# Optimization experiments

Measured on AMD Instinct MI355X. Metric: run time of the kernel, lower is better.

Reference implementation:

```python
import jax, jax.numpy as jnp
import numpy as np

D_IN = 1024
D_OUT = 1024

def setup_inputs() -> dict:
    key = jax.random.key(0)
    ks = jax.random.split(key, 7)
    s = 1.0 / np.sqrt(D_IN)
    x = jax.random.normal(ks[0], (4, 2048, D_IN), dtype=jnp.float32)
    Wq = jax.random.uniform(ks[1], (D_IN, D_OUT), jnp.float32, -s, s)
    Wk = jax.random.uniform(ks[2], (D_IN, D_OUT), jnp.float32, -s, s)
    Wv = jax.random.uniform(ks[3], (D_IN, D_OUT), jnp.float32, -s, s)
    bq = jax.random.uniform(ks[4], (D_OUT,), jnp.float32, -s, s)
    bk = jax.random.uniform(ks[5], (D_OUT,), jnp.float32, -s, s)
    bv = jax.random.uniform(ks[6], (D_OUT,), jnp.float32, -s, s)
    return {"x": x, "Wq": Wq, "Wk": Wk, "Wv": Wv, "bq": bq, "bk": bk, "bv": bv}

def reference(x, Wq, Wk, Wv, bq, bk, bv):
    # x: [b, n, d_in]
    q = jnp.einsum('bnd,de->bne', x, Wq) + bq
    k = jnp.einsum('bnd,de->bne', x, Wk) + bk
    v = jnp.einsum('bnd,de->bne', x, Wv) + bv
    scale = 1.0 / jnp.sqrt(jnp.asarray(k.shape[-1], dtype=x.dtype))
    scores = jnp.einsum('bqe,bke->bqk', q, k) * scale  # [b, n, n]
    weights = jax.nn.softmax(scores, axis=-1)
    return jnp.einsum('bqk,bke->bqe', weights, v)
```

## Files before the change

### kernel.cpp

```cpp
#include <hip/hip_runtime.h>
#include <cstdint>

typedef __bf16 bf16x8 __attribute__((ext_vector_type(8)));
typedef float f32x4 __attribute__((ext_vector_type(4)));

__device__ __forceinline__ unsigned short f2b(float f) {
    union { float f; uint32_t u; } x; x.f = f;
    uint32_t r = (x.u + 0x7fffu + ((x.u >> 16) & 1u)) >> 16;
    return (unsigned short)r;
}
__device__ __forceinline__ float b2f(unsigned short h) {
    union { float f; uint32_t u; } x; x.u = ((uint32_t)h) << 16;
    return x.f;
}

__global__ __launch_bounds__(256) void convert_x_kernel(const float* __restrict__ x,
                                                        unsigned short* __restrict__ xb) {
    int i = (blockIdx.x * 256 + threadIdx.x) * 4;
    float4 v = *(const float4*)(x + i);
    ushort4 o;
    o.x = f2b(v.x); o.y = f2b(v.y); o.z = f2b(v.z); o.w = f2b(v.w);
    *(ushort4*)(xb + i) = o;
}

__global__ __launch_bounds__(1024) void transpose_w_kernel(const float* __restrict__ Wq,
                                                           const float* __restrict__ Wk,
                                                           const float* __restrict__ Wv,
                                                           unsigned short* __restrict__ Wt) {
    __shared__ float tile[32][33];
    const float* W = (blockIdx.z == 0) ? Wq : (blockIdx.z == 1) ? Wk : Wv;
    int n0 = blockIdx.x * 32, k0 = blockIdx.y * 32;
    int tx = threadIdx.x, ty = threadIdx.y;
    tile[ty][tx] = W[(k0 + ty) * 1024 + n0 + tx];
    __syncthreads();
    Wt[((long)blockIdx.z * 1024 + n0 + ty) * 1024 + k0 + tx] = f2b(tile[tx][ty]);
}

template <int EPI>
__global__ __launch_bounds__(256) void gemm_bt(const unsigned short* __restrict__ A, int lda, long sA,
                                               const unsigned short* __restrict__ Bm, int ldb, long sB,
                                               void* __restrict__ Cv, long sC, int K,
                                               const float* __restrict__ bq, const float* __restrict__ bk,
                                               const float* __restrict__ bv,
                                               unsigned short* __restrict__ Qb,
                                               unsigned short* __restrict__ Kb,
                                               unsigned short* __restrict__ Vt) {
    __shared__ unsigned short As[128 * 32];
    __shared__ unsigned short Bs[128 * 32];

    const int tid = threadIdx.x;
    const int wave = tid >> 6, lane = tid & 63;
    const int quad = lane >> 4, c16 = lane & 15;
    const int wm = wave >> 1, wn = wave & 1;
    const long bm = (long)blockIdx.y * 128;
    const long bn = (long)blockIdx.x * 128;

    const unsigned short* Ab = A + (long)blockIdx.z * sA;
    const unsigned short* Bb = Bm + (long)blockIdx.z * sB;

    f32x4 acc[4][4];
#pragma unroll
    for (int mi = 0; mi < 4; ++mi)
#pragma unroll
        for (int ni = 0; ni < 4; ++ni)
#pragma unroll
            for (int r = 0; r < 4; ++r) acc[mi][ni][r] = 0.0f;

    const int srow = wave * 16 + (lane >> 2);
    const int skk = (lane & 3) * 8;
    const unsigned short* aptr0 = Ab + (bm + srow) * (long)lda + skk;
    const unsigned short* aptr1 = aptr0 + 64L * lda;
    const unsigned short* bptr0 = Bb + (bn + srow) * (long)ldb + skk;
    const unsigned short* bptr1 = bptr0 + 64L * ldb;
    unsigned short* asl0 = &As[(wave * 16) * 32];
    unsigned short* asl1 = &As[(64 + wave * 16) * 32];
    unsigned short* bsl0 = &Bs[(wave * 16) * 32];
    unsigned short* bsl1 = &Bs[(64 + wave * 16) * 32];

    for (int k0 = 0; k0 < K; k0 += 32) {
        __builtin_amdgcn_global_load_lds((const __attribute__((address_space(1))) void*)(aptr0 + k0),
                                         (__attribute__((address_space(3))) void*)asl0, 16, 0, 0);
        __builtin_amdgcn_global_load_lds((const __attribute__((address_space(1))) void*)(aptr1 + k0),
                                         (__attribute__((address_space(3))) void*)asl1, 16, 0, 0);
        __builtin_amdgcn_global_load_lds((const __attribute__((address_space(1))) void*)(bptr0 + k0),
                                         (__attribute__((address_space(3))) void*)bsl0, 16, 0, 0);
        __builtin_amdgcn_global_load_lds((const __attribute__((address_space(1))) void*)(bptr1 + k0),
                                         (__attribute__((address_space(3))) void*)bsl1, 16, 0, 0);
        __syncthreads();

        bf16x8 af[4], bf[4];
#pragma unroll
        for (int mi = 0; mi < 4; ++mi)
            af[mi] = *(const bf16x8*)&As[(wm * 64 + mi * 16 + c16) * 32 + quad * 8];
#pragma unroll
        for (int ni = 0; ni < 4; ++ni)
            bf[ni] = *(const bf16x8*)&Bs[(wn * 64 + ni * 16 + c16) * 32 + quad * 8];
#pragma unroll
        for (int mi = 0; mi < 4; ++mi)
#pragma unroll
            for (int ni = 0; ni < 4; ++ni)
                acc[mi][ni] = __builtin_amdgcn_mfma_f32_16x16x32_bf16(af[mi], bf[ni], acc[mi][ni], 0, 0, 0);
        __syncthreads();
    }

#pragma unroll
    for (int mi = 0; mi < 4; ++mi) {
        const long row0 = bm + wm * 64 + mi * 16 + quad * 4;
#pragma unroll
        for (int ni = 0; ni < 4; ++ni) {
            const int col = (int)bn + wn * 64 + ni * 16 + c16;
            if constexpr (EPI == 0) {
                if (col < 1024) {
                    const float bias = bq[col];
#pragma unroll
                    for (int r = 0; r < 4; ++r)
                        Qb[(row0 + r) * 1024 + col] = f2b((acc[mi][ni][r] + bias) * 0.03125f);
                } else if (col < 2048) {
                    const float bias = bk[col - 1024];
#pragma unroll
                    for (int r = 0; r < 4; ++r)
                        Kb[(row0 + r) * 1024 + (col - 1024)] = f2b(acc[mi][ni][r] + bias);
                } else {
                    const float bias = bv[col - 2048];
                    const long batch = row0 >> 11;
                    const int n = (int)(row0 & 2047);
                    ushort4 o;
                    o.x = f2b(acc[mi][ni][0] + bias);
                    o.y = f2b(acc[mi][ni][1] + bias);
                    o.z = f2b(acc[mi][ni][2] + bias);
                    o.w = f2b(acc[mi][ni][3] + bias);
                    *(ushort4*)&Vt[((batch << 10) + (col - 2048)) * 2048L + n] = o;
                }
            } else if constexpr (EPI == 1) {
                unsigned short* S = (unsigned short*)Cv + (long)blockIdx.z * sC;
#pragma unroll
                for (int r = 0; r < 4; ++r)
                    S[(row0 + r) * 2048 + col] = f2b(acc[mi][ni][r]);
            } else {
                float* O = (float*)Cv + (long)blockIdx.z * sC;
#pragma unroll
                for (int r = 0; r < 4; ++r)
                    O[(row0 + r) * 1024 + col] = acc[mi][ni][r];
            }
        }
    }
}

__global__ __launch_bounds__(256) void softmax_kernel(unsigned short* __restrict__ S) {
    const long row = blockIdx.x;
    unsigned short* p = S + row * 2048;
    const int tid = threadIdx.x;
    const int wave = tid >> 6, lane = tid & 63;

    ushort4 u0 = *(const ushort4*)&p[tid * 8];
    ushort4 u1 = *(const ushort4*)&p[tid * 8 + 4];
    float v[8];
    v[0] = b2f(u0.x); v[1] = b2f(u0.y); v[2] = b2f(u0.z); v[3] = b2f(u0.w);
    v[4] = b2f(u1.x); v[5] = b2f(u1.y); v[6] = b2f(u1.z); v[7] = b2f(u1.w);

    float m = v[0];
#pragma unroll
    for (int j = 1; j < 8; ++j) m = fmaxf(m, v[j]);
#pragma unroll
    for (int off = 32; off; off >>= 1) m = fmaxf(m, __shfl_xor(m, off, 64));
    __shared__ float redm[4];
    __shared__ float reds[4];
    if (lane == 0) redm[wave] = m;
    __syncthreads();
    m = fmaxf(fmaxf(redm[0], redm[1]), fmaxf(redm[2], redm[3]));

    float s = 0.0f;
#pragma unroll
    for (int j = 0; j < 8; ++j) { v[j] = __expf(v[j] - m); s += v[j]; }
#pragma unroll
    for (int off = 32; off; off >>= 1) s += __shfl_xor(s, off, 64);
    if (lane == 0) reds[wave] = s;
    __syncthreads();
    s = reds[0] + reds[1] + reds[2] + reds[3];
    const float inv = 1.0f / s;

    u0.x = f2b(v[0] * inv); u0.y = f2b(v[1] * inv); u0.z = f2b(v[2] * inv); u0.w = f2b(v[3] * inv);
    u1.x = f2b(v[4] * inv); u1.y = f2b(v[5] * inv); u1.z = f2b(v[6] * inv); u1.w = f2b(v[7] * inv);
    *(ushort4*)&p[tid * 8] = u0;
    *(ushort4*)&p[tid * 8 + 4] = u1;
}

extern "C" void kernel_launch(void* const* d_in, const int* in_sizes, int n_in,
                              void* d_out, int out_size, void* d_ws, size_t ws_size,
                              hipStream_t stream) {
    const float* x  = (const float*)d_in[0];
    const float* Wq = (const float*)d_in[1];
    const float* Wk = (const float*)d_in[2];
    const float* Wv = (const float*)d_in[3];
    const float* bq = (const float*)d_in[4];
    const float* bk = (const float*)d_in[5];
    const float* bv = (const float*)d_in[6];
    float* out = (float*)d_out;

    char* ws = (char*)d_ws;
    unsigned short* xb = (unsigned short*)ws; ws += 8192L * 1024 * 2;
    unsigned short* Wt = (unsigned short*)ws; ws += 3072L * 1024 * 2;
    unsigned short* Qb = (unsigned short*)ws; ws += 8192L * 1024 * 2;
    unsigned short* Kb = (unsigned short*)ws; ws += 8192L * 1024 * 2;
    unsigned short* Vt = (unsigned short*)ws; ws += 4L * 1024 * 2048 * 2;
    unsigned short* S  = (unsigned short*)ws; ws += 4L * 2048 * 2048 * 2;

    convert_x_kernel<<<8192, 256, 0, stream>>>(x, xb);
    transpose_w_kernel<<<dim3(32, 32, 3), dim3(32, 32), 0, stream>>>(Wq, Wk, Wv, Wt);
    gemm_bt<0><<<dim3(24, 64, 1), 256, 0, stream>>>(xb, 1024, 0, Wt, 1024, 0,
                                                    nullptr, 0, 1024, bq, bk, bv, Qb, Kb, Vt);
    gemm_bt<1><<<dim3(16, 16, 4), 256, 0, stream>>>(Qb, 1024, 2048L * 1024, Kb, 1024, 2048L * 1024,
                                                    S, 2048L * 2048, 1024,
                                                    nullptr, nullptr, nullptr, nullptr, nullptr, nullptr);
    softmax_kernel<<<8192, 256, 0, stream>>>(S);
    gemm_bt<2><<<dim3(8, 16, 4), 256, 0, stream>>>(S, 2048, 2048L * 2048, Vt, 2048, 2048L * 1024,
                                                   out, 2048L * 1024, 2048,
                                                   nullptr, nullptr, nullptr, nullptr, nullptr, nullptr);
}
```

Measured before the change: 307.4 us.

## Switch GEMMs to 32x32x16 MFMA with K=64 tiles and XOR-swizzled LDS

```diff
diff --git a/kernel.cpp b/kernel.cpp
--- a/kernel.cpp
+++ b/kernel.cpp
@@ -2,7 +2,7 @@
 #include <cstdint>
 
 typedef __bf16 bf16x8 __attribute__((ext_vector_type(8)));
-typedef float f32x4 __attribute__((ext_vector_type(4)));
+typedef float f32x16 __attribute__((ext_vector_type(16)));
 
 __device__ __forceinline__ unsigned short f2b(float f) {
     union { float f; uint32_t u; } x; x.f = f;
@@ -37,20 +37,21 @@
 }
 
 template <int EPI>
-__global__ __launch_bounds__(256) void gemm_bt(const unsigned short* __restrict__ A, int lda, long sA,
-                                               const unsigned short* __restrict__ Bm, int ldb, long sB,
-                                               void* __restrict__ Cv, long sC, int K,
-                                               const float* __restrict__ bq, const float* __restrict__ bk,
-                                               const float* __restrict__ bv,
-                                               unsigned short* __restrict__ Qb,
-                                               unsigned short* __restrict__ Kb,
-                                               unsigned short* __restrict__ Vt) {
-    __shared__ unsigned short As[128 * 32];
-    __shared__ unsigned short Bs[128 * 32];
+__global__ __launch_bounds__(256) void gemm32(const unsigned short* __restrict__ A, int lda, long sA,
+                                              const unsigned short* __restrict__ Bm, int ldb, long sB,
+                                              void* __restrict__ Cv, long sC, int K,
+                                              const float* __restrict__ bq, const float* __restrict__ bk,
+                                              const float* __restrict__ bv,
+                                              unsigned short* __restrict__ Qb,
+                                              unsigned short* __restrict__ Kb,
+                                              unsigned short* __restrict__ Vt) {
+    __shared__ unsigned short As[128 * 64];
+    __shared__ unsigned short Bs[128 * 64];
 
     const int tid = threadIdx.x;
     const int wave = tid >> 6, lane = tid & 63;
-    const int quad = lane >> 4, c16 = lane & 15;
+    const int h = lane >> 5;
+    const int l31 = lane & 31;
     const int wm = wave >> 1, wn = wave & 1;
     const long bm = (long)blockIdx.y * 128;
     const long bn = (long)blockIdx.x * 128;
@@ -58,89 +59,122 @@
     const unsigned short* Ab = A + (long)blockIdx.z * sA;
     const unsigned short* Bb = Bm + (long)blockIdx.z * sB;
 
-    f32x4 acc[4][4];
-#pragma unroll
-    for (int mi = 0; mi < 4; ++mi)
-#pragma unroll
-        for (int ni = 0; ni < 4; ++ni)
-#pragma unroll
-            for (int r = 0; r < 4; ++r) acc[mi][ni][r] = 0.0f;
-
-    const int srow = wave * 16 + (lane >> 2);
-    const int skk = (lane & 3) * 8;
-    const unsigned short* aptr0 = Ab + (bm + srow) * (long)lda + skk;
-    const unsigned short* aptr1 = aptr0 + 64L * lda;
-    const unsigned short* bptr0 = Bb + (bn + srow) * (long)ldb + skk;
-    const unsigned short* bptr1 = bptr0 + 64L * ldb;
-    unsigned short* asl0 = &As[(wave * 16) * 32];
-    unsigned short* asl1 = &As[(64 + wave * 16) * 32];
-    unsigned short* bsl0 = &Bs[(wave * 16) * 32];
-    unsigned short* bsl1 = &Bs[(64 + wave * 16) * 32];
-
-    for (int k0 = 0; k0 < K; k0 += 32) {
-        __builtin_amdgcn_global_load_lds((const __attribute__((address_space(1))) void*)(aptr0 + k0),
-                                         (__attribute__((address_space(3))) void*)asl0, 16, 0, 0);
-        __builtin_amdgcn_global_load_lds((const __attribute__((address_space(1))) void*)(aptr1 + k0),
-                                         (__attribute__((address_space(3))) void*)asl1, 16, 0, 0);
-        __builtin_amdgcn_global_load_lds((const __attribute__((address_space(1))) void*)(bptr0 + k0),
-                                         (__attribute__((address_space(3))) void*)bsl0, 16, 0, 0);
-        __builtin_amdgcn_global_load_lds((const __attribute__((address_space(1))) void*)(bptr1 + k0),
-                                         (__attribute__((address_space(3))) void*)bsl1, 16, 0, 0);
+    f32x16 acc[2][2];
+#pragma unroll
+    for (int mi = 0; mi < 2; ++mi)
+#pragma unroll
+        for (int ni = 0; ni < 2; ++ni)
+#pragma unroll
+            for (int r = 0; r < 16; ++r) acc[mi][ni][r] = 0.0f;
+
+    const int srow_in = lane >> 3;
+    const int cswz = (lane & 7) ^ srow_in;
+    const unsigned short* aptr[4];
+    const unsigned short* bptr[4];
+    unsigned short* asl[4];
+    unsigned short* bsl[4];
+#pragma unroll
+    for (int j = 0; j < 4; ++j) {
+        const int row = j * 32 + wave * 8 + srow_in;
+        aptr[j] = Ab + (bm + row) * (long)lda + cswz * 8;
+        bptr[j] = Bb + (bn + row) * (long)ldb + cswz * 8;
+        asl[j] = &As[(j * 32 + wave * 8) * 64];
+        bsl[j] = &Bs[(j * 32 + wave * 8) * 64];
+    }
+
+    const int arow0 = (wm * 64 + l31) * 64;
+    const int brow0 = (wn * 64 + l31) * 64;
+    int sw[4];
+#pragma unroll
+    for (int kh = 0; kh < 4; ++kh)
+        sw[kh] = (((2 * kh + h) ^ (lane & 7)) * 8);
+
+    for (int k0 = 0; k0 < K; k0 += 64) {
+#pragma unroll
+        for (int j = 0; j < 4; ++j) {
+            __builtin_amdgcn_global_load_lds((const __attribute__((address_space(1))) void*)(aptr[j] + k0),
+                                             (__attribute__((address_space(3))) void*)asl[j], 16, 0, 0);
+            __builtin_amdgcn_global_load_lds((const __attribute__((address_space(1))) void*)(bptr[j] + k0),
+                                             (__attribute__((address_space(3))) void*)bsl[j], 16, 0, 0);
+        }
         __syncthreads();
 
-        bf16x8 af[4], bf[4];
-#pragma unroll
-        for (int mi = 0; mi < 4; ++mi)
-            af[mi] = *(const bf16x8*)&As[(wm * 64 + mi * 16 + c16) * 32 + quad * 8];
-#pragma unroll
-        for (int ni = 0; ni < 4; ++ni)
-            bf[ni] = *(const bf16x8*)&Bs[(wn * 64 + ni * 16 + c16) * 32 + quad * 8];
-#pragma unroll
-        for (int mi = 0; mi < 4; ++mi)
-#pragma unroll
-            for (int ni = 0; ni < 4; ++ni)
-                acc[mi][ni] = __builtin_amdgcn_mfma_f32_16x16x32_bf16(af[mi], bf[ni], acc[mi][ni], 0, 0, 0);
+#pragma unroll
+        for (int kp = 0; kp < 2; ++kp) {
+            bf16x8 af[2][2], bfr[2][2];
+#pragma unroll
+            for (int mi = 0; mi < 2; ++mi)
+#pragma unroll
+                for (int kk = 0; kk < 2; ++kk)
+                    af[mi][kk] = *(const bf16x8*)&As[arow0 + mi * 32 * 64 + sw[kp * 2 + kk]];
+#pragma unroll
+            for (int ni = 0; ni < 2; ++ni)
+#pragma unroll
+                for (int kk = 0; kk < 2; ++kk)
+                    bfr[ni][kk] = *(const bf16x8*)&Bs[brow0 + ni * 32 * 64 + sw[kp * 2 + kk]];
+#pragma unroll
+            for (int kk = 0; kk < 2; ++kk)
+#pragma unroll
+                for (int mi = 0; mi < 2; ++mi)
+#pragma unroll
+                    for (int ni = 0; ni < 2; ++ni)
+                        acc[mi][ni] = __builtin_amdgcn_mfma_f32_32x32x16_bf16(af[mi][kk], bfr[ni][kk],
+                                                                              acc[mi][ni], 0, 0, 0);
+        }
         __syncthreads();
     }
 
 #pragma unroll
-    for (int mi = 0; mi < 4; ++mi) {
-        const long row0 = bm + wm * 64 + mi * 16 + quad * 4;
-#pragma unroll
-        for (int ni = 0; ni < 4; ++ni) {
-            const int col = (int)bn + wn * 64 + ni * 16 + c16;
+    for (int mi = 0; mi < 2; ++mi) {
+#pragma unroll
+        for (int ni = 0; ni < 2; ++ni) {
+            const f32x16 a = acc[mi][ni];
+            const long col = bn + wn * 64 + ni * 32 + l31;
+            const long rowB = bm + wm * 64 + mi * 32 + h * 4;
             if constexpr (EPI == 0) {
                 if (col < 1024) {
                     const float bias = bq[col];
 #pragma unroll
-                    for (int r = 0; r < 4; ++r)
-                        Qb[(row0 + r) * 1024 + col] = f2b((acc[mi][ni][r] + bias) * 0.03125f);
+                    for (int g = 0; g < 4; ++g)
+#pragma unroll
+                        for (int r = 0; r < 4; ++r)
+                            Qb[(rowB + g * 8 + r) * 1024 + col] = f2b((a[g * 4 + r] + bias) * 0.03125f);
                 } else if (col < 2048) {
                     const float bias = bk[col - 1024];
 #pragma unroll
-                    for (int r = 0; r < 4; ++r)
-                        Kb[(row0 + r) * 1024 + (col - 1024)] = f2b(acc[mi][ni][r] + bias);
+                    for (int g = 0; g < 4; ++g)
+#pragma unroll
+                        for (int r = 0; r < 4; ++r)
+                            Kb[(rowB + g * 8 + r) * 1024 + (col - 1024)] = f2b(a[g * 4 + r] + bias);
                 } else {
                     const float bias = bv[col - 2048];
-                    const long batch = row0 >> 11;
-                    const int n = (int)(row0 & 2047);
-                    ushort4 o;
-                    o.x = f2b(acc[mi][ni][0] + bias);
-                    o.y = f2b(acc[mi][ni][1] + bias);
-                    o.z = f2b(acc[mi][ni][2] + bias);
-                    o.w = f2b(acc[mi][ni][3] + bias);
-                    *(ushort4*)&Vt[((batch << 10) + (col - 2048)) * 2048L + n] = o;
+#pragma unroll
+                    for (int g = 0; g < 4; ++g) {
+                        const long row0 = rowB + g * 8;
+                        const long batch = row0 >> 11;
+                        const int n = (int)(row0 & 2047);
+                        ushort4 o;
+                        o.x = f2b(a[g * 4 + 0] + bias);
+                        o.y = f2b(a[g * 4 + 1] + bias);
+                        o.z = f2b(a[g * 4 + 2] + bias);
+                        o.w = f2b(a[g * 4 + 3] + bias);
+                        *(ushort4*)&Vt[(batch * 1024 + (col - 2048)) * 2048 + n] = o;
+                    }
                 }
             } else if constexpr (EPI == 1) {
                 unsigned short* S = (unsigned short*)Cv + (long)blockIdx.z * sC;
 #pragma unroll
-                for (int r = 0; r < 4; ++r)
-                    S[(row0 + r) * 2048 + col] = f2b(acc[mi][ni][r]);
+                for (int g = 0; g < 4; ++g)
+#pragma unroll
+                    for (int r = 0; r < 4; ++r)
+                        S[(rowB + g * 8 + r) * 2048 + col] = f2b(a[g * 4 + r]);
             } else {
                 float* O = (float*)Cv + (long)blockIdx.z * sC;
 #pragma unroll
-                for (int r = 0; r < 4; ++r)
-                    O[(row0 + r) * 1024 + col] = acc[mi][ni][r];
+                for (int g = 0; g < 4; ++g)
+#pragma unroll
+                    for (int r = 0; r < 4; ++r)
+                        O[(rowB + g * 8 + r) * 1024 + col] = a[g * 4 + r];
             }
         }
     }
@@ -207,13 +241,13 @@
 
     convert_x_kernel<<<8192, 256, 0, stream>>>(x, xb);
     transpose_w_kernel<<<dim3(32, 32, 3), dim3(32, 32), 0, stream>>>(Wq, Wk, Wv, Wt);
-    gemm_bt<0><<<dim3(24, 64, 1), 256, 0, stream>>>(xb, 1024, 0, Wt, 1024, 0,
-                                                    nullptr, 0, 1024, bq, bk, bv, Qb, Kb, Vt);
-    gemm_bt<1><<<dim3(16, 16, 4), 256, 0, stream>>>(Qb, 1024, 2048L * 1024, Kb, 1024, 2048L * 1024,
-                                                    S, 2048L * 2048, 1024,
-                                                    nullptr, nullptr, nullptr, nullptr, nullptr, nullptr);
+    gemm32<0><<<dim3(24, 64, 1), 256, 0, stream>>>(xb, 1024, 0, Wt, 1024, 0,
+                                                   nullptr, 0, 1024, bq, bk, bv, Qb, Kb, Vt);
+    gemm32<1><<<dim3(16, 16, 4), 256, 0, stream>>>(Qb, 1024, 2048L * 1024, Kb, 1024, 2048L * 1024,
+                                                   S, 2048L * 2048, 1024,
+                                                   nullptr, nullptr, nullptr, nullptr, nullptr, nullptr);
     softmax_kernel<<<8192, 256, 0, stream>>>(S);
-    gemm_bt<2><<<dim3(8, 16, 4), 256, 0, stream>>>(S, 2048, 2048L * 2048, Vt, 2048, 2048L * 1024,
-                                                   out, 2048L * 1024, 2048,
-                                                   nullptr, nullptr, nullptr, nullptr, nullptr, nullptr);
-}
+    gemm32<2><<<dim3(8, 16, 4), 256, 0, stream>>>(S, 2048, 2048L * 2048, Vt, 2048, 2048L * 1024,
+                                                  out, 2048L * 1024, 2048,
+                                                  nullptr, nullptr, nullptr, nullptr, nullptr, nullptr);
+}
```

New measurement: 279.9 us. -8.9%, faster.
